# Optimization experiments

Measured on AMD Instinct MI355X. Metric: run time of the kernel, lower is better.

## Reference

```python
import jax, jax.numpy as jnp
import numpy as np

B, F, D = 1024, 39, 64
UNITS = [128, 128, 128]


def setup_inputs() -> dict:
    key = jax.random.key(0)
    ks = jax.random.split(key, 7)
    X_0 = jax.random.normal(ks[0], (B, F, D), dtype=jnp.float32)
    in_ch = [F * F, F * UNITS[0], F * UNITS[1]]
    out = {"X_0": X_0}
    for i, (ic, oc) in enumerate(zip(in_ch, UNITS)):
        bound = float(1.0 / np.sqrt(ic))  # torch Conv1d default init bound
        out[f"W{i+1}"] = jax.random.uniform(ks[1 + 2 * i], (oc, ic), minval=-bound, maxval=bound, dtype=jnp.float32)
        out[f"b{i+1}"] = jax.random.uniform(ks[2 + 2 * i], (oc,), minval=-bound, maxval=bound, dtype=jnp.float32)
    return out


def reference(X_0, W1, b1, W2, b2, W3, b3):
    # X_0: [B, F, D]
    bsz, _, d = X_0.shape
    X_i = X_0
    pooled = []
    for W, b in ((W1, b1), (W2, b2), (W3, b3)):
        # outer-product interaction: [B, F, M, D] -> [B, F*M, D]
        had = jnp.einsum('bhd,bmd->bhmd', X_0, X_i).reshape(bsz, -1, d)
        # 1x1 conv == channel matmul: [B, C, D] x [O, C] -> [B, O, D]
        X_i = jnp.einsum('bcd,oc->bod', had, W) + b[None, :, None]
        pooled.append(X_i.sum(axis=-1))  # sum-pool over embedding dim -> [B, O]
    return jnp.concatenate(pooled, axis=-1)  # [B, sum(UNITS)]
```

## Files before the change

kernel.cpp:

```cpp
#include <hip/hip_runtime.h>
#include <stdint.h>


#define F_N 39
#define D_N 64
#define O_N 128

typedef _Float16 f16;
typedef _Float16 f16x8 __attribute__((ext_vector_type(8)));
typedef _Float16 f16x4 __attribute__((ext_vector_type(4)));
typedef float f32x4 __attribute__((ext_vector_type(4)));

__device__ __forceinline__ unsigned short h2u(f16 h) {
  union { f16 h; unsigned short u; } v; v.h = h; return v.u;
}

__device__ __forceinline__ void repack_one(const float* __restrict__ w,
                                           f16* __restrict__ y, int idx,
                                           int KS, int Mv, int RS) {
  int j = idx & 7, lane = (idx >> 3) & 63, p = (idx >> 9) & 1, wv = (idx >> 10) & 3;
  int kkh = idx >> 12, kk = kkh % KS, h = kkh / KS;
  int o = wv * 32 + p * 16 + (lane & 15);
  int m = kk * 32 + (lane >> 4) * 8 + j;
  y[idx] = (m < Mv) ? (f16)w[(size_t)o * RS + h * Mv + m] : (f16)0.f;
}

__global__ __launch_bounds__(256) void prep_k(const float* __restrict__ W1,
                                              const float* __restrict__ W2,
                                              const float* __restrict__ W3,
                                              f16* __restrict__ W1f,
                                              f16* __restrict__ W2f,
                                              f16* __restrict__ W3f) {
  int blk = blockIdx.x, t = threadIdx.x;
  if (blk < 1248) {
    repack_one(W1, W1f, blk * 256 + t, 2, 39, 1521);
  } else if (blk < 3744) {
    repack_one(W2, W2f, (blk - 1248) * 256 + t, 4, 128, 4992);
  } else {
    repack_one(W3, W3f, (blk - 3744) * 256 + t, 156, 4992, 4992);
  }
}

template <int KS>
__device__ __forceinline__ void layer_mm(const f16* __restrict__ Wf_base,
                                         const unsigned short* xi_t,
                                         const f16* x0s,
                                         f32x4 (&accO)[2][4],
                                         int wave, int lane, int lr, int lg) {
  constexpr int MP = KS * 32;
  f16x8 bbr[KS][4];
  #pragma unroll
  for (int kk = 0; kk < KS; ++kk)
    #pragma unroll
    for (int nf = 0; nf < 4; ++nf) {
      const int n = nf * 16 + lr;
      const int off = (n * (MP * 2) + (kk * 32 + lg * 8) * 2) ^ ((n & 7) << 4);
      bbr[kk][nf] = *(const f16x8*)((const char*)xi_t + off);
    }
  __syncthreads();

  const f16x8* Wf = (const f16x8*)Wf_base;
  const int wbase = wave * 128 + lane;
  f16x8 wA[KS][2], wB[KS][2];

  auto loadW = [&](f16x8 (&buf)[KS][2], int hh) {
    const f16x8* pw = Wf + (size_t)hh * (KS * 512) + wbase;
    #pragma unroll
    for (int kk = 0; kk < KS; ++kk)
      #pragma unroll
      for (int p = 0; p < 2; ++p)
        buf[kk][p] = pw[kk * 512 + p * 64];
  };

  auto body = [&](f16x8 (&buf)[KS][2], int h) {
    f16 sv[4];
    #pragma unroll
    for (int nf = 0; nf < 4; ++nf) sv[nf] = x0s[h * 64 + nf * 16 + lr];
    #pragma unroll
    for (int kk = 0; kk < KS; ++kk)
      #pragma unroll
      for (int nf = 0; nf < 4; ++nf) {
        f16x8 sb = bbr[kk][nf] * sv[nf];
        accO[0][nf] = __builtin_amdgcn_mfma_f32_16x16x32_f16(buf[kk][0], sb, accO[0][nf], 0, 0, 0);
        accO[1][nf] = __builtin_amdgcn_mfma_f32_16x16x32_f16(buf[kk][1], sb, accO[1][nf], 0, 0, 0);
      }
  };

  loadW(wA, 0);
  for (int h = 0; h < F_N; h += 2) {
    loadW(wB, (h + 1 < F_N) ? h + 1 : F_N - 1);
    body(wA, h);
    loadW(wA, (h + 2 < F_N) ? h + 2 : F_N - 1);
    if (h + 1 < F_N) body(wB, h + 1);
  }
}

__global__ __launch_bounds__(256, 2) void cin_fused_k(
    const float* __restrict__ X0f,
    const f16* __restrict__ W1f,
    const f16* __restrict__ W2f,
    const float* __restrict__ b1,
    const float* __restrict__ b2,
    f16* __restrict__ Gb,
    float* __restrict__ out)
{
  __shared__ __align__(16) unsigned short xi_t[8192];
  __shared__ f16 x0s[48 * 64];
  __shared__ float pld[2][128];

  const int b = blockIdx.x, t = threadIdx.x;
  const int wave = t >> 6, lane = t & 63, lr = lane & 15, lg = lane >> 4;
  const f32x4 zero4 = {0.f, 0.f, 0.f, 0.f};
  const float* xs = X0f + (size_t)b * (F_N * D_N);

  {
    const int d = t & 63, m0 = t >> 6;
    #pragma unroll
    for (int m = m0; m < 64; m += 4) {
      f16 v = (m < F_N) ? (f16)xs[m * 64 + d] : (f16)0.f;
      int off = (d * 128 + m * 2) ^ ((d & 7) << 4);
      *(unsigned short*)((char*)xi_t + off) = h2u(v);
    }
    for (int i = t; i < 3072; i += 256)
      x0s[i] = (i < F_N * D_N) ? (f16)xs[i] : (f16)0.f;
  }
  __syncthreads();

  f32x4 accO[2][4];
  #pragma unroll
  for (int p = 0; p < 2; ++p)
    #pragma unroll
    for (int nf = 0; nf < 4; ++nf) accO[p][nf] = zero4;
  layer_mm<2>(W1f, xi_t, x0s, accO, wave, lane, lr, lg);

  {
    float bv[2][4];
    #pragma unroll
    for (int p = 0; p < 2; ++p)
      #pragma unroll
      for (int r = 0; r < 4; ++r) bv[p][r] = b1[wave * 32 + p * 16 + lg * 4 + r];

    #pragma unroll
    for (int p = 0; p < 2; ++p)
      #pragma unroll
      for (int nf = 0; nf < 4; ++nf)
        #pragma unroll
        for (int r = 0; r < 4; ++r) {
          int o = wave * 32 + p * 16 + lg * 4 + r;
          int d = nf * 16 + lr;
          f16 val = (f16)(accO[p][nf][r] + bv[p][r]);
          int off = (d * 256 + o * 2) ^ ((d & 7) << 4);
          *(unsigned short*)((char*)xi_t + off) = h2u(val);
        }

    #pragma unroll
    for (int p = 0; p < 2; ++p)
      #pragma unroll
      for (int r = 0; r < 4; ++r) {
        float v = accO[p][0][r] + accO[p][1][r] + accO[p][2][r] + accO[p][3][r];
        v += __shfl_xor(v, 1, 16);
        v += __shfl_xor(v, 2, 16);
        v += __shfl_xor(v, 4, 16);
        v += __shfl_xor(v, 8, 16);
        if (lr == 0) pld[0][wave * 32 + p * 16 + lg * 4 + r] = v;
      }
  }
  __syncthreads();
  if (t < 128) out[(size_t)b * 384 + t] = pld[0][t] + 64.0f * b1[t];

  #pragma unroll
  for (int p = 0; p < 2; ++p)
    #pragma unroll
    for (int nf = 0; nf < 4; ++nf) accO[p][nf] = zero4;
  layer_mm<4>(W2f, xi_t, x0s, accO, wave, lane, lr, lg);

  {
    float bv[2][4];
    #pragma unroll
    for (int p = 0; p < 2; ++p)
      #pragma unroll
      for (int r = 0; r < 4; ++r) bv[p][r] = b2[wave * 32 + p * 16 + lg * 4 + r];

    #pragma unroll
    for (int p = 0; p < 2; ++p)
      #pragma unroll
      for (int nf = 0; nf < 4; ++nf)
        #pragma unroll
        for (int r = 0; r < 4; ++r) {
          int o = wave * 32 + p * 16 + lg * 4 + r;
          int d = nf * 16 + lr;
          xi_t[o * 64 + d] = h2u((f16)(accO[p][nf][r] + bv[p][r]));
        }

    #pragma unroll
    for (int p = 0; p < 2; ++p)
      #pragma unroll
      for (int r = 0; r < 4; ++r) {
        float v = accO[p][0][r] + accO[p][1][r] + accO[p][2][r] + accO[p][3][r];
        v += __shfl_xor(v, 1, 16);
        v += __shfl_xor(v, 2, 16);
        v += __shfl_xor(v, 4, 16);
        v += __shfl_xor(v, 8, 16);
        if (lr == 0) pld[1][wave * 32 + p * 16 + lg * 4 + r] = v;
      }
  }
  __syncthreads();
  if (t < 128) out[(size_t)b * 384 + 128 + t] = pld[1][t] + 64.0f * b2[t];

  {
    const f16* x2 = (const f16*)xi_t;
    f16x8 af[3][2], bfr[2][2];
    #pragma unroll
    for (int hf = 0; hf < 3; ++hf)
      #pragma unroll
      for (int kk = 0; kk < 2; ++kk)
        af[hf][kk] = *(const f16x8*)(x0s + (hf * 16 + lr) * 64 + kk * 32 + lg * 8);
    #pragma unroll
    for (int mf = 0; mf < 2; ++mf)
      #pragma unroll
      for (int kk = 0; kk < 2; ++kk)
        bfr[mf][kk] = *(const f16x8*)(x2 + (wave * 32 + mf * 16 + lr) * 64 + kk * 32 + lg * 8);

    f32x4 acc[3][2];
    #pragma unroll
    for (int hf = 0; hf < 3; ++hf)
      #pragma unroll
      for (int mf = 0; mf < 2; ++mf) {
        acc[hf][mf] = __builtin_amdgcn_mfma_f32_16x16x32_f16(af[hf][0], bfr[mf][0], zero4, 0, 0, 0);
        acc[hf][mf] = __builtin_amdgcn_mfma_f32_16x16x32_f16(af[hf][1], bfr[mf][1], acc[hf][mf], 0, 0, 0);
      }

    #pragma unroll
    for (int hf = 0; hf < 3; ++hf)
      #pragma unroll
      for (int mf = 0; mf < 2; ++mf)
        #pragma unroll
        for (int r = 0; r < 4; ++r) {
          int h = hf * 16 + lg * 4 + r;
          if (h < F_N)
            Gb[(size_t)b * 4992 + h * 128 + wave * 32 + mf * 16 + lr] = (f16)acc[hf][mf][r];
        }
  }
}

__global__ __launch_bounds__(256) void pooled3_k(
    const f16* __restrict__ Gb,
    const f16* __restrict__ W3f,
    const float* __restrict__ b3,
    float* __restrict__ out)
{
  const int b0 = blockIdx.x * 16, t = threadIdx.x;
  const int wave = t >> 6, lane = t & 63, lr = lane & 15, lg = lane >> 4;
  const f32x4 zero4 = {0.f, 0.f, 0.f, 0.f};

  const f16* ga = Gb + (size_t)(b0 + lr) * 4992 + lg * 8;
  const f16x8* wf = (const f16x8*)W3f;
  const int wbase = wave * 128 + lane;

  f32x4 acc0 = zero4, acc1 = zero4;
  #pragma unroll 4
  for (int ks = 0; ks < 156; ++ks) {
    f16x8 a  = *(const f16x8*)(ga + ks * 32);
    f16x8 q0 = wf[ks * 512 + wbase];
    f16x8 q1 = wf[ks * 512 + wbase + 64];
    acc0 = __builtin_amdgcn_mfma_f32_16x16x32_f16(a, q0, acc0, 0, 0, 0);
    acc1 = __builtin_amdgcn_mfma_f32_16x16x32_f16(a, q1, acc1, 0, 0, 0);
  }

  #pragma unroll
  for (int r = 0; r < 4; ++r) {
    int bb = b0 + lg * 4 + r;
    int o0 = wave * 32 + lr;
    out[(size_t)bb * 384 + 256 + o0]      = acc0[r] + 64.0f * b3[o0];
    out[(size_t)bb * 384 + 256 + o0 + 16] = acc1[r] + 64.0f * b3[o0 + 16];
  }
}

extern "C" void kernel_launch(void* const* d_in, const int* in_sizes, int n_in,
                              void* d_out, int out_size, void* d_ws, size_t ws_size,
                              hipStream_t stream) {
  const float* X0 = (const float*)d_in[0];
  const float* W1 = (const float*)d_in[1];
  const float* b1 = (const float*)d_in[2];
  const float* W2 = (const float*)d_in[3];
  const float* b2 = (const float*)d_in[4];
  const float* W3 = (const float*)d_in[5];
  const float* b3 = (const float*)d_in[6];
  float* out = (float*)d_out;

  f16* W1f = (f16*)d_ws;
  f16* W2f = W1f + 319488;
  f16* W3f = W2f + 638976;
  f16* Gb  = W3f + 638976;

  prep_k<<<6240, 256, 0, stream>>>(W1, W2, W3, W1f, W2f, W3f);
  cin_fused_k<<<1024, 256, 0, stream>>>(X0, W1f, W2f, b1, b2, Gb, out);
  pooled3_k<<<64, 256, 0, stream>>>(Gb, W3f, b3, out);
}
```

Before: 253.9 us.

## Split pooled3 GEMM across output groups and K-slices with shared-memory reduction

```diff
diff --git a/kernel.cpp b/kernel.cpp
--- a/kernel.cpp
+++ b/kernel.cpp
@@ -249,30 +249,43 @@
     const float* __restrict__ b3,
     float* __restrict__ out)
 {
-  const int b0 = blockIdx.x * 16, t = threadIdx.x;
+  __shared__ float red[3][64][4];
+  const int bg = blockIdx.x >> 3, og = blockIdx.x & 7;
+  const int t = threadIdx.x;
   const int wave = t >> 6, lane = t & 63, lr = lane & 15, lg = lane >> 4;
   const f32x4 zero4 = {0.f, 0.f, 0.f, 0.f};
+  const int b0 = bg * 16;
 
   const f16* ga = Gb + (size_t)(b0 + lr) * 4992 + lg * 8;
   const f16x8* wf = (const f16x8*)W3f;
-  const int wbase = wave * 128 + lane;
-
-  f32x4 acc0 = zero4, acc1 = zero4;
-  #pragma unroll 4
-  for (int ks = 0; ks < 156; ++ks) {
-    f16x8 a  = *(const f16x8*)(ga + ks * 32);
-    f16x8 q0 = wf[ks * 512 + wbase];
-    f16x8 q1 = wf[ks * 512 + wbase + 64];
-    acc0 = __builtin_amdgcn_mfma_f32_16x16x32_f16(a, q0, acc0, 0, 0, 0);
-    acc1 = __builtin_amdgcn_mfma_f32_16x16x32_f16(a, q1, acc1, 0, 0, 0);
-  }
-
-  #pragma unroll
-  for (int r = 0; r < 4; ++r) {
-    int bb = b0 + lg * 4 + r;
-    int o0 = wave * 32 + lr;
-    out[(size_t)bb * 384 + 256 + o0]      = acc0[r] + 64.0f * b3[o0];
-    out[(size_t)bb * 384 + 256 + o0 + 16] = acc1[r] + 64.0f * b3[o0 + 16];
+  const int wbase = og * 64 + lane;
+  const int ks0 = wave * 39;
+
+  f32x4 acc = zero4;
+  #pragma unroll 3
+  for (int i = 0; i < 39; ++i) {
+    const int ks = ks0 + i;
+    f16x8 a = *(const f16x8*)(ga + ks * 32);
+    f16x8 q = wf[(size_t)ks * 512 + wbase];
+    acc = __builtin_amdgcn_mfma_f32_16x16x32_f16(a, q, acc, 0, 0, 0);
+  }
+
+  if (wave > 0) {
+    #pragma unroll
+    for (int r = 0; r < 4; ++r) red[wave - 1][lane][r] = acc[r];
+  }
+  __syncthreads();
+  if (wave == 0) {
+    #pragma unroll
+    for (int w = 0; w < 3; ++w)
+      #pragma unroll
+      for (int r = 0; r < 4; ++r) acc[r] += red[w][lane][r];
+    const int o = og * 16 + lr;
+    #pragma unroll
+    for (int r = 0; r < 4; ++r) {
+      int bb = b0 + lg * 4 + r;
+      out[(size_t)bb * 384 + 256 + o] = acc[r] + 64.0f * b3[o];
+    }
   }
 }
 
@@ -295,5 +308,5 @@
 
   prep_k<<<6240, 256, 0, stream>>>(W1, W2, W3, W1f, W2f, W3f);
   cin_fused_k<<<1024, 256, 0, stream>>>(X0, W1f, W2f, b1, b2, Gb, out);
-  pooled3_k<<<64, 256, 0, stream>>>(Gb, W3f, b3, out);
-}
+  pooled3_k<<<512, 256, 0, stream>>>(Gb, W3f, b3, out);
+}
```

Result: faster. 218.8 us (-13.8%).
